# Optimization experiments

Hardware: AMD Instinct MI355X
Metric: run time of the kernel (lower is better)

Reference implementation:

```python
import jax, jax.numpy as jnp
import numpy as np

N, E, G = 50000, 800000, 64
F_IN, H, R, C = 64, 64, 3, 10


def setup_inputs() -> dict:
    key = jax.random.key(0)
    ks = jax.random.split(key, 16)
    s = 0.1
    return dict(
        x=jax.random.normal(ks[0], (N, F_IN), jnp.float32),
        edge_index=jax.random.randint(ks[1], (2, E), 0, N, dtype=jnp.int32),
        edge_type=jax.random.randint(ks[2], (E,), 0, R, dtype=jnp.int32),
        graph_batch=jnp.sort(jax.random.randint(ks[3], (N,), 0, G, dtype=jnp.int32)),
        # FiLMConv params (per-relation lin: bias=False; per-relation film: bias=True)
        film_lin_W=jax.random.normal(ks[4], (R, F_IN, H), jnp.float32) * s,
        film_film_W=jax.random.normal(ks[5], (R, F_IN, 2 * H), jnp.float32) * s,
        film_film_b=jnp.zeros((R, 2 * H), jnp.float32),
        skip_W=jax.random.normal(ks[6], (F_IN, H), jnp.float32) * s,
        skip_film_W=jax.random.normal(ks[7], (F_IN, 2 * H), jnp.float32) * s,
        skip_film_b=jnp.zeros((2 * H,), jnp.float32),
        # GATConv params (heads=1, concat=True, lin bias=False, final bias=True)
        gat_W=jax.random.normal(ks[8], (F_IN, H), jnp.float32) * s,
        gat_att_src=jax.random.normal(ks[9], (H,), jnp.float32) * s,
        gat_att_dst=jax.random.normal(ks[10], (H,), jnp.float32) * s,
        gat_b=jnp.zeros((H,), jnp.float32),
        # classifier MLP
        lin_W=jax.random.normal(ks[11], (4 * H, H), jnp.float32) * s,
        lin_b=jnp.zeros((H,), jnp.float32),
        fc_W=jax.random.normal(ks[12], (H, C), jnp.float32) * s,
        fc_b=jnp.zeros((C,), jnp.float32),
    )


def _film_conv(x, edge_index, edge_type, lin_W, film_W, film_b,
               skip_W, skip_film_W, skip_film_b):
    # PyG FiLMConv, aggr='mean' per relation, act=relu.
    n, r, h = x.shape[0], lin_W.shape[0], skip_W.shape[1]
    src, dst = edge_index[0], edge_index[1]
    fs = x @ skip_film_W + skip_film_b                  # [N,2H]; split -> (beta, gamma)
    out = jax.nn.relu(fs[:, h:] * (x @ skip_W) + fs[:, :h])
    xr = jnp.einsum('nd,rdh->rnh', x, lin_W)            # [R,N,H]
    fm = jnp.einsum('nd,rdh->rnh', x, film_W) + film_b[:, None, :]  # [R,N,2H]
    beta, gamma = fm[..., :h], fm[..., h:]
    # each edge uses its own relation's lin/film params
    msg = jax.nn.relu(gamma[edge_type, dst] * xr[edge_type, src] + beta[edge_type, dst])  # [E,H]
    seg = dst * r + edge_type                            # per-(node,relation) mean
    cnt = jax.ops.segment_sum(jnp.ones_like(msg[:, 0]), seg, num_segments=n * r)
    denom = jnp.maximum(cnt[seg], 1.0)
    agg = jax.ops.segment_sum(msg / denom[:, None], dst, num_segments=n)
    return out + agg


def _gat_conv(x, edge_index, W, att_src, att_dst, b):
    # PyG GATConv, heads=1, negative_slope=0.2, add_self_loops=True.
    n = x.shape[0]
    xp = x @ W                                           # [N,H]
    loop = jnp.arange(n, dtype=edge_index.dtype)
    src = jnp.concatenate([edge_index[0], loop])
    dst = jnp.concatenate([edge_index[1], loop])
    e = jax.nn.leaky_relu((xp @ att_src)[src] + (xp @ att_dst)[dst], 0.2)  # [E+N]
    m = jax.ops.segment_max(e, dst, num_segments=n)
    alpha = jnp.exp(e - m[dst])
    denom = jax.ops.segment_sum(alpha, dst, num_segments=n)
    alpha = alpha / denom[dst]
    return jax.ops.segment_sum(alpha[:, None] * xp[src], dst, num_segments=n) + b


def reference(x, edge_index, edge_type, graph_batch,
              film_lin_W, film_film_W, film_film_b, skip_W, skip_film_W, skip_film_b,
              gat_W, gat_att_src, gat_att_dst, gat_b,
              lin_W, lin_b, fc_W, fc_b):
    out1 = jax.nn.relu(_film_conv(x, edge_index, edge_type, film_lin_W, film_film_W,
                                  film_film_b, skip_W, skip_film_W, skip_film_b))
    out2 = jax.nn.relu(_gat_conv(x, edge_index, gat_W, gat_att_src, gat_att_dst, gat_b))
    feats = jnp.concatenate([out1, out2], axis=-1)       # [N,2H]
    g = G
    cnt = jax.ops.segment_sum(jnp.ones_like(feats[:, 0]), graph_batch, num_segments=g)
    mx = jax.ops.segment_max(feats, graph_batch, num_segments=g)
    mx = jnp.where(cnt[:, None] > 0, mx, 0.0)
    mean = jax.ops.segment_sum(feats, graph_batch, num_segments=g) / jnp.maximum(cnt, 1.0)[:, None]
    pooled = jnp.concatenate([mx, mean], axis=-1)        # [G,4H]
    hidden = jax.nn.relu(pooled @ lin_W + lin_b)         # dropout = identity (eval)
    logits = hidden @ fc_W + fc_b
    return jax.nn.log_softmax(logits, axis=-1)
```

## Files before the change

### kernel.cpp

```cpp
#include <hip/hip_runtime.h>
#include <hip/hip_bf16.h>

#define NN 50000
#define EE 800000
#define GG 64
#define RR 3
#define CC 10
#define RPL 16
#define CAP 96

typedef __attribute__((ext_vector_type(8))) short bf16x8;
typedef __attribute__((ext_vector_type(4))) float f32x4;

__device__ inline float leaky02(float x) { return x > 0.f ? x : 0.2f * x; }

__device__ inline void atomicMaxFPos(float* addr, float v) {
  atomicMax((int*)addr, __float_as_int(v));
}

__device__ inline unsigned short f2bf(float f) {
  __hip_bfloat16 b = __float2bfloat16(f);
  return *reinterpret_cast<unsigned short*>(&b);
}
__device__ inline float bf2f(unsigned short u) {
  return __uint_as_float(((unsigned int)u) << 16);
}

__global__ void scat_k(const int* __restrict__ ei, const int* __restrict__ et,
                       int* __restrict__ fill, int* __restrict__ sorted,
                       const float* __restrict__ skip_film_W,
                       const float* __restrict__ skip_W,
                       const float* __restrict__ film_lin_W,
                       const float* __restrict__ film_film_W,
                       const float* __restrict__ gat_W,
                       const float* __restrict__ skip_film_b,
                       const float* __restrict__ film_film_b,
                       unsigned short* __restrict__ Wt,
                       float* __restrict__ bias) {
  int b = blockIdx.x;
  if (b < 3125) {
    int e = b * 256 + threadIdx.x;
    int src = ei[e], dst = ei[EE + e], t = et[e];
    int slot = atomicAdd(&fill[dst], 1);
    if (slot < CAP) sorted[dst * CAP + slot] = src | (t << 20);
    return;
  }
  int idx = (b - 3125) * 256 + threadIdx.x;
  if (idx >= 832 * 64 + 832) return;
  if (idx >= 832 * 64) {
    int c = idx - 832 * 64;
    float bv = 0.f;
    if (c < 128) bv = skip_film_b[c];
    else if (c >= 384 && c < 768) bv = film_film_b[c - 384];
    bias[c] = bv;
    return;
  }
  int c = idx >> 6, k = idx & 63;
  float v;
  if (c < 128)      v = skip_film_W[k * 128 + c];
  else if (c < 192) v = skip_W[k * 64 + (c - 128)];
  else if (c < 384) { int cc = c - 192, r = cc >> 6, h = cc & 63;
                      v = film_lin_W[(r * 64 + k) * 64 + h]; }
  else if (c < 768) { int cc = c - 384, r = cc >> 7, j = cc & 127;
                      v = film_film_W[(r * 64 + k) * 128 + j]; }
  else              v = gat_W[k * 64 + (c - 768)];
  Wt[idx] = f2bf(v);
}

__global__ __launch_bounds__(256) void gemm_k(const float* __restrict__ X,
    const unsigned short* __restrict__ Wt, const float* __restrict__ bias,
    const float* __restrict__ att_src, const float* __restrict__ att_dst,
    unsigned short* __restrict__ Z, unsigned short* __restrict__ Ybg,
    unsigned short* __restrict__ S0b, float* __restrict__ as_,
    float* __restrict__ ad_) {
  __shared__ __align__(16) unsigned short As[64][72];
  __shared__ __align__(16) unsigned short Bs[128][72];
  const int tid = threadIdx.x;
  const int row0 = blockIdx.x * 64;

  {
    int r = tid >> 2, c0 = (tid & 3) * 16;
    int gr = row0 + r;
    ushort4 o0 = {0,0,0,0}, o1 = {0,0,0,0}, o2 = {0,0,0,0}, o3 = {0,0,0,0};
    if (gr < NN) {
      const float4* p = reinterpret_cast<const float4*>(X + (size_t)gr * 64 + c0);
      float4 v0 = p[0], v1 = p[1], v2 = p[2], v3 = p[3];
      o0 = {f2bf(v0.x), f2bf(v0.y), f2bf(v0.z), f2bf(v0.w)};
      o1 = {f2bf(v1.x), f2bf(v1.y), f2bf(v1.z), f2bf(v1.w)};
      o2 = {f2bf(v2.x), f2bf(v2.y), f2bf(v2.z), f2bf(v2.w)};
      o3 = {f2bf(v3.x), f2bf(v3.y), f2bf(v3.z), f2bf(v3.w)};
    }
    *reinterpret_cast<ushort4*>(&As[r][c0])      = o0;
    *reinterpret_cast<ushort4*>(&As[r][c0 + 4])  = o1;
    *reinterpret_cast<ushort4*>(&As[r][c0 + 8])  = o2;
    *reinterpret_cast<ushort4*>(&As[r][c0 + 12]) = o3;
  }
  __syncthreads();

  const int w = tid >> 6, lane = tid & 63;
  const int m = lane & 15, q = lane >> 4;
  bf16x8 a0 = *reinterpret_cast<const bf16x8*>(&As[16 * w + m][q * 8]);
  bf16x8 a1 = *reinterpret_cast<const bf16x8*>(&As[16 * w + m][32 + q * 8]);
  const int rbase = row0 + 16 * w + q * 4;

  unsigned short* Z0 = Z;
  unsigned short* Z1 = Z + (size_t)NN * 128;
  unsigned short* Z2 = Z + (size_t)NN * 256;

  f32x4 t0[8], t1[4], t6[4];

  for (int tile = 0; tile < 7; tile++) {
    __syncthreads();
    int col0 = tile * 128;
    int width = (tile == 6) ? 64 : 128;
    {
      int c = tid >> 1, half = (tid & 1) * 32;
      if (c < width) {
        int gc = col0 + c;
        const uint4* p = reinterpret_cast<const uint4*>(Wt + (size_t)gc * 64 + half);
        uint4 v0 = p[0], v1 = p[1], v2 = p[2], v3 = p[3];
        *reinterpret_cast<uint4*>(&Bs[c][half])      = v0;
        *reinterpret_cast<uint4*>(&Bs[c][half + 8])  = v1;
        *reinterpret_cast<uint4*>(&Bs[c][half + 16]) = v2;
        *reinterpret_cast<uint4*>(&Bs[c][half + 24]) = v3;
      }
    }
    __syncthreads();
    #pragma unroll
    for (int ct = 0; ct < 8; ct++) {
      if (tile == 6 && ct >= 4) continue;
      bf16x8 b0 = *reinterpret_cast<const bf16x8*>(&Bs[ct * 16 + m][q * 8]);
      bf16x8 b1 = *reinterpret_cast<const bf16x8*>(&Bs[ct * 16 + m][32 + q * 8]);
      f32x4 acc = {0.f, 0.f, 0.f, 0.f};
      acc = __builtin_amdgcn_mfma_f32_16x16x32_bf16(a0, b0, acc, 0, 0, 0);
      acc = __builtin_amdgcn_mfma_f32_16x16x32_bf16(a1, b1, acc, 0, 0, 0);
      if (tile == 0) { t0[ct] = acc; continue; }
      if (tile == 1 && ct < 4) { t1[ct] = acc; continue; }
      if (tile == 6) t6[ct] = acc;
      int colm = ct * 16 + m;
      float bv = (tile >= 3 && tile <= 5) ? bias[col0 + colm] : 0.f;
      #pragma unroll
      for (int rg = 0; rg < 4; rg++) {
        int gr = rbase + rg;
        if (gr >= NN) continue;
        float v = acc[rg];
        if (tile == 1) {
          Z0[(size_t)gr * 128 + colm] = f2bf(v);
        } else if (tile == 2) {
          if (ct < 4) Z1[(size_t)gr * 128 + 64 + colm] = f2bf(v);
          else        Z2[(size_t)gr * 128 + colm]      = f2bf(v);
        } else if (tile <= 5) {
          Ybg[(size_t)gr * 384 + (col0 - 384) + colm] = f2bf(v + bv);
        } else {
          unsigned short b16 = f2bf(v);
          Z0[(size_t)gr * 128 + colm] = b16;
          Z1[(size_t)gr * 128 + colm] = b16;
          Z2[(size_t)gr * 128 + colm] = b16;
        }
      }
    }
  }

  float pa[4] = {0.f, 0.f, 0.f, 0.f}, pd[4] = {0.f, 0.f, 0.f, 0.f};
  #pragma unroll
  for (int j = 0; j < 4; j++) {
    int h = 16 * j + m;
    float bb = bias[h];
    float bg = bias[64 + h];
    float asv = att_src[h];
    float adv = att_dst[h];
    #pragma unroll
    for (int rg = 0; rg < 4; rg++) {
      float so = fmaxf((t0[4 + j][rg] + bg) * t1[j][rg] + (t0[j][rg] + bb), 0.f);
      int gr = rbase + rg;
      if (gr < NN) S0b[(size_t)gr * 64 + h] = f2bf(so);
      pa[rg] += t6[j][rg] * asv;
      pd[rg] += t6[j][rg] * adv;
    }
  }
  #pragma unroll
  for (int ofs = 1; ofs < 16; ofs <<= 1) {
    #pragma unroll
    for (int rg = 0; rg < 4; rg++) {
      pa[rg] += __shfl_xor(pa[rg], ofs);
      pd[rg] += __shfl_xor(pd[rg], ofs);
    }
  }
  if (m == 0) {
    #pragma unroll
    for (int rg = 0; rg < 4; rg++) {
      int gr = rbase + rg;
      if (gr < NN) { as_[gr] = pa[rg]; ad_[gr] = pd[rg]; }
    }
  }
}

#define RPN 16

__global__ __launch_bounds__(256) void dst_k(const int* __restrict__ sorted,
    const int* __restrict__ fill, const unsigned short* __restrict__ Z,
    const unsigned short* __restrict__ Ybg,
    const unsigned short* __restrict__ S0b,
    const float* __restrict__ as_, const float* __restrict__ ad_,
    const float* __restrict__ gat_b, const int* __restrict__ gb,
    float* __restrict__ pmax, float* __restrict__ psum,
    int* __restrict__ gstart, int* __restrict__ gend) {
  __shared__ int s_wpk[8 * CAP];
  __shared__ __align__(16) unsigned short s_rows[64][128];
  __shared__ int s_deg[4], s_g[4];
  __shared__ float s_ad[4];
  float* s_val = (float*)&s_rows[0][0];

  int tid = threadIdx.x;
  int wid = tid >> 6, h = tid & 63;
  int n0 = blockIdx.x * 4;
  int n = n0 + wid;

  size_t rep = (size_t)(blockIdx.x & (RPL - 1)) * GG * 128;
  pmax += rep; psum += rep;

  if (h == 0) {
    int d = fill[n]; if (d > CAP) d = CAP;
    s_deg[wid] = d;
    s_g[wid] = gb[n];
    s_ad[wid] = ad_[n];
  }
  __syncthreads();

  for (int i = tid; i < 4 * CAP; i += 256) {
    int wd = i / CAP, j = i - wd * CAP;
    if (j < s_deg[wd]) {
      int pk = sorted[(size_t)(n0 + wd) * CAP + j];
      int s = pk & 0xFFFFF;
      float e = leaky02(as_[s] + s_ad[wd]);
      s_wpk[2 * i]     = pk;
      s_wpk[2 * i + 1] = __float_as_int(e);
    }
  }
  __syncthreads();

  int mydeg = s_deg[wid];
  float adn = s_ad[wid];
  float es = leaky02(as_[n] + adn);
  int base = wid * CAP;

  float e1 = -1e30f, e2 = -1e30f;
  int pk1 = -1, pk2 = -1;
  if (h < mydeg) {
    pk1 = s_wpk[2 * (base + h)];
    e1  = __int_as_float(s_wpk[2 * (base + h) + 1]);
  }
  if (h + 64 < mydeg) {
    pk2 = s_wpk[2 * (base + 64 + h)];
    e2  = __int_as_float(s_wpk[2 * (base + 64 + h) + 1]);
  }
  float mg = fmaxf(fmaxf(e1, e2), es);
  #pragma unroll
  for (int ofs = 1; ofs < 64; ofs <<= 1) mg = fmaxf(mg, __shfl_xor(mg, ofs));
  float w1 = (h < mydeg)      ? __expf(e1 - mg) : 0.f;
  float w2 = (h + 64 < mydeg) ? __expf(e2 - mg) : 0.f;
  if (h < mydeg)      s_wpk[2 * (base + h) + 1]      = __float_as_int(w1);
  if (h + 64 < mydeg) s_wpk[2 * (base + 64 + h) + 1] = __float_as_int(w2);
  float den = w1 + w2;
  #pragma unroll
  for (int ofs = 1; ofs < 64; ofs <<= 1) den += __shfl_xor(den, ofs);
  float ws = __expf(es - mg);
  den += ws;

  int t1v = pk1 >> 20, t2v = pk2 >> 20;
  int c0 = __popcll(__ballot(t1v == 0)) + __popcll(__ballot(t2v == 0));
  int c1 = __popcll(__ballot(t1v == 1)) + __popcll(__ballot(t2v == 1));
  int c2 = __popcll(__ballot(t1v == 2)) + __popcll(__ballot(t2v == 2));
  float i0 = 1.f / (float)(c0 > 1 ? c0 : 1);
  float i1 = 1.f / (float)(c1 > 1 ? c1 : 1);
  float i2 = 1.f / (float)(c2 > 1 ? c2 : 1);

  const unsigned short* ybg = Ybg + (size_t)n * 384;
  float b0p = bf2f(ybg[h])       * i0, g0p = bf2f(ybg[64 + h])  * i0;
  float b1p = bf2f(ybg[128 + h]) * i1, g1p = bf2f(ybg[192 + h]) * i1;
  float b2p = bf2f(ybg[256 + h]) * i2, g2p = bf2f(ybg[320 + h]) * i2;

  float S = ws * bf2f(Z[(size_t)n * 128 + h]);
  float f = 0.f;

  const int grp16 = tid >> 4, lane16 = tid & 15;
  int dmax = max(max(s_deg[0], s_deg[1]), max(s_deg[2], s_deg[3]));
  int rounds = (dmax + RPN - 1) / RPN;

  for (int r = 0; r < rounds; r++) {
    int e0 = r * RPN;
    #pragma unroll
    for (int k = 0; k < 4; k++) {
      int slot = grp16 + 16 * k;
      int wd = slot >> 4, j = slot & 15;
      int jj = e0 + j;
      if (jj < s_deg[wd]) {
        int pk = s_wpk[2 * (wd * CAP + jj)];
        int src = pk & 0xFFFFF;
        int t = pk >> 20;
        const unsigned short* row = Z + ((size_t)t * NN + src) * 128;
        uint4 v = *reinterpret_cast<const uint4*>(row + lane16 * 8);
        *reinterpret_cast<uint4*>(&s_rows[slot][lane16 * 8]) = v;
      }
    }
    __syncthreads();
    int cn = mydeg - e0; if (cn > RPN) cn = RPN;
    const int* wp = &s_wpk[2 * (base + e0)];
    const unsigned short* rowp = &s_rows[wid * RPN][0];
    for (int j = 0; j < cn; j++) {
      int pkj  = wp[2 * j];
      float wj = __int_as_float(wp[2 * j + 1]);
      int tj = pkj >> 20;
      float xp = bf2f(rowp[j * 128 + h]);
      float xr = bf2f(rowp[j * 128 + 64 + h]);
      S += wj * xp;
      float gt = tj == 0 ? g0p : (tj == 1 ? g1p : g2p);
      float bt = tj == 0 ? b0p : (tj == 1 ? b1p : b2p);
      f += fmaxf(gt * xr + bt, 0.f);
    }
    __syncthreads();
  }

  float o1 = fmaxf(bf2f(S0b[(size_t)n * 64 + h]) + f, 0.f);
  float o2 = fmaxf(S / den + gat_b[h], 0.f);

  s_val[wid * 128 + h]      = o1;
  s_val[wid * 128 + 64 + h] = o2;
  if (h == 0) {
    int g = s_g[wid];
    if (n == 0 || gb[n - 1] != g)      gstart[g] = n;
    if (n == NN - 1 || gb[n + 1] != g) gend[g] = n;
  }
  __syncthreads();
  if (tid < 128) {
    int fch = tid;
    int curg = s_g[0];
    float v0 = s_val[fch];
    float mx = v0, sm = v0;
    #pragma unroll
    for (int j = 1; j < 4; j++) {
      float v = s_val[j * 128 + fch];
      if (s_g[j] == curg) { mx = fmaxf(mx, v); sm += v; }
      else {
        atomicMaxFPos(&pmax[curg * 128 + fch], mx);
        atomicAdd(&psum[curg * 128 + fch], sm);
        curg = s_g[j]; mx = v; sm = v;
      }
    }
    atomicMaxFPos(&pmax[curg * 128 + fch], mx);
    atomicAdd(&psum[curg * 128 + fch], sm);
  }
}

__global__ __launch_bounds__(64) void head_k(const float* __restrict__ pmax,
    const float* __restrict__ psum, const int* __restrict__ gstart,
    const int* __restrict__ gend,
    const float* __restrict__ lin_W, const float* __restrict__ lin_b,
    const float* __restrict__ fc_W, const float* __restrict__ fc_b,
    float* __restrict__ out) {
  __shared__ float p[256];
  __shared__ float hid[64];
  __shared__ float lg[CC];
  __shared__ float lse;
  int g = blockIdx.x, t = threadIdx.x;
  int s = gstart[g], e = gend[g];
  int cnt = (s <= e && s < NN && s >= 0) ? (e - s + 1) : 0;
  float invc = 1.f / (float)(cnt > 1 ? cnt : 1);
  for (int i = t; i < 256; i += 64) {
    if (i < 128) {
      float mx = 0.f;
      for (int r = 0; r < RPL; r++)
        mx = fmaxf(mx, pmax[((size_t)r * GG + g) * 128 + i]);
      p[i] = mx;
    } else {
      int f = i - 128;
      float sm = 0.f;
      for (int r = 0; r < RPL; r++)
        sm += psum[((size_t)r * GG + g) * 128 + f];
      p[i] = sm * invc;
    }
  }
  __syncthreads();
  float acc = lin_b[t];
  for (int k = 0; k < 256; k++) acc += p[k] * lin_W[k * 64 + t];
  hid[t] = fmaxf(acc, 0.f);
  __syncthreads();
  if (t < CC) {
    float a = fc_b[t];
    for (int k = 0; k < 64; k++) a += hid[k] * fc_W[k * CC + t];
    lg[t] = a;
  }
  __syncthreads();
  if (t == 0) {
    float mx = lg[0];
    for (int i = 1; i < CC; i++) mx = fmaxf(mx, lg[i]);
    float sum = 0.f;
    for (int i = 0; i < CC; i++) sum += expf(lg[i] - mx);
    lse = mx + logf(sum);
  }
  __syncthreads();
  if (t < CC) out[g * CC + t] = lg[t] - lse;
}

extern "C" void kernel_launch(void* const* d_in, const int* in_sizes, int n_in,
                              void* d_out, int out_size, void* d_ws, size_t ws_size,
                              hipStream_t stream) {
  const float* x            = (const float*)d_in[0];
  const int*   edge_index   = (const int*)d_in[1];
  const int*   edge_type    = (const int*)d_in[2];
  const int*   graph_batch  = (const int*)d_in[3];
  const float* film_lin_W   = (const float*)d_in[4];
  const float* film_film_W  = (const float*)d_in[5];
  const float* film_film_b  = (const float*)d_in[6];
  const float* skip_W       = (const float*)d_in[7];
  const float* skip_film_W  = (const float*)d_in[8];
  const float* skip_film_b  = (const float*)d_in[9];
  const float* gat_W        = (const float*)d_in[10];
  const float* att_src      = (const float*)d_in[11];
  const float* att_dst      = (const float*)d_in[12];
  const float* gat_b        = (const float*)d_in[13];
  const float* lin_W        = (const float*)d_in[14];
  const float* lin_b        = (const float*)d_in[15];
  const float* fc_W         = (const float*)d_in[16];
  const float* fc_b         = (const float*)d_in[17];
  float* out                = (float*)d_out;

  float* ws = (float*)d_ws;
  const size_t N = NN, G = GG;
  size_t oZ      = 0;
  size_t oYbg    = N * 192;
  size_t oS0     = oYbg + N * 192;
  size_t oAs     = oS0 + N * 32;
  size_t oAd     = oAs + N;
  size_t oWt     = oAd + N;
  size_t oBias   = oWt + 832 * 32;
  size_t oPmax   = oBias + 832;
  size_t oPsum   = oPmax + (size_t)RPL * G * 128;
  size_t oGend   = oPsum + (size_t)RPL * G * 128;
  size_t oFill   = oGend + G;
  size_t oGstart = oFill + N;
  size_t oSorted = oGstart + G;

  unsigned short* Z   = (unsigned short*)(ws + oZ);
  unsigned short* Ybg = (unsigned short*)(ws + oYbg);
  unsigned short* S0b = (unsigned short*)(ws + oS0);
  float* as_    = ws + oAs;
  float* ad_    = ws + oAd;
  unsigned short* Wt  = (unsigned short*)(ws + oWt);
  float* bias   = ws + oBias;
  float* pmax   = ws + oPmax;
  float* psum   = ws + oPsum;
  int*   gend   = (int*)(ws + oGend);
  int*   fill   = (int*)(ws + oFill);
  int*   gstart = (int*)(ws + oGstart);
  int*   sorted = (int*)(ws + oSorted);

  size_t zeroFloats = oGstart - oPmax;
  hipMemsetAsync(pmax, 0, zeroFloats * sizeof(float), stream);

  scat_k<<<3125 + 210, 256, 0, stream>>>(edge_index, edge_type, fill, sorted,
      skip_film_W, skip_W, film_lin_W, film_film_W, gat_W,
      skip_film_b, film_film_b, Wt, bias);
  gemm_k<<<(NN + 63) / 64, 256, 0, stream>>>(x, Wt, bias, att_src, att_dst,
                                             Z, Ybg, S0b, as_, ad_);
  dst_k<<<NN / 4, 256, 0, stream>>>(sorted, fill, Z, Ybg, S0b, as_, ad_,
                                    gat_b, graph_batch, pmax, psum,
                                    gstart, gend);
  head_k<<<GG, 64, 0, stream>>>(pmax, psum, gstart, gend,
                                lin_W, lin_b, fc_W, fc_b, out);
}
```

Measured before the change: 248.6 us.

## Bucket edges by relation per destination and double-buffer neighbor row gathers

The edge scatter now bins each destination's incoming edges into three per-relation buckets of 32 slots, with a counter per (node, relation). Per-relation counts therefore come straight from those counters, which removes the ballot/popcount passes and the per-edge relation select in the inner loop. The dst kernel also double-buffers the shared-memory row tiles, loading the next round's neighbor rows into registers while the current round is processed, so there is one barrier per round instead of two. This doubles the shared staging buffer and adds register pressure. Capping each relation at 32 edges changes overflow behaviour compared with the single 96-slot cap.

```diff
diff --git a/kernel.cpp b/kernel.cpp
--- a/kernel.cpp
+++ b/kernel.cpp
@@ -27,7 +27,7 @@
 }
 
 __global__ void scat_k(const int* __restrict__ ei, const int* __restrict__ et,
-                       int* __restrict__ fill, int* __restrict__ sorted,
+                       int* __restrict__ fill4, int* __restrict__ sorted,
                        const float* __restrict__ skip_film_W,
                        const float* __restrict__ skip_W,
                        const float* __restrict__ film_lin_W,
@@ -41,8 +41,8 @@
   if (b < 3125) {
     int e = b * 256 + threadIdx.x;
     int src = ei[e], dst = ei[EE + e], t = et[e];
-    int slot = atomicAdd(&fill[dst], 1);
-    if (slot < CAP) sorted[dst * CAP + slot] = src | (t << 20);
+    int slot = atomicAdd(&fill4[dst * 4 + t], 1);
+    if (slot < 32) sorted[dst * 96 + t * 32 + slot] = src;
     return;
   }
   int idx = (b - 3125) * 256 + threadIdx.x;
@@ -198,128 +198,164 @@
 #define RPN 16
 
 __global__ __launch_bounds__(256) void dst_k(const int* __restrict__ sorted,
-    const int* __restrict__ fill, const unsigned short* __restrict__ Z,
+    const int* __restrict__ fill4, const unsigned short* __restrict__ Z,
     const unsigned short* __restrict__ Ybg,
     const unsigned short* __restrict__ S0b,
     const float* __restrict__ as_, const float* __restrict__ ad_,
     const float* __restrict__ gat_b, const int* __restrict__ gb,
     float* __restrict__ pmax, float* __restrict__ psum,
     int* __restrict__ gstart, int* __restrict__ gend) {
-  __shared__ int s_wpk[8 * CAP];
-  __shared__ __align__(16) unsigned short s_rows[64][128];
-  __shared__ int s_deg[4], s_g[4];
+  __shared__ int   s_pk[4][96];
+  __shared__ float s_w [4][96];
+  __shared__ int   s_d [4][4];
+  __shared__ int   s_g[4];
   __shared__ float s_ad[4];
-  float* s_val = (float*)&s_rows[0][0];
-
-  int tid = threadIdx.x;
-  int wid = tid >> 6, h = tid & 63;
-  int n0 = blockIdx.x * 4;
-  int n = n0 + wid;
+  __shared__ __align__(16) unsigned short s_rows[2][64][128];
+  float* s_val = (float*)&s_rows[0][0][0];
+
+  const int tid = threadIdx.x;
+  const int wid = tid >> 6, h = tid & 63;
+  const int n0 = blockIdx.x * 4;
+  const int n  = n0 + wid;
 
   size_t rep = (size_t)(blockIdx.x & (RPL - 1)) * GG * 128;
   pmax += rep; psum += rep;
 
-  if (h == 0) {
-    int d = fill[n]; if (d > CAP) d = CAP;
-    s_deg[wid] = d;
-    s_g[wid] = gb[n];
-    s_ad[wid] = ad_[n];
-  }
-  __syncthreads();
-
-  for (int i = tid; i < 4 * CAP; i += 256) {
-    int wd = i / CAP, j = i - wd * CAP;
-    if (j < s_deg[wd]) {
-      int pk = sorted[(size_t)(n0 + wd) * CAP + j];
-      int s = pk & 0xFFFFF;
-      float e = leaky02(as_[s] + s_ad[wd]);
-      s_wpk[2 * i]     = pk;
-      s_wpk[2 * i + 1] = __float_as_int(e);
-    }
-  }
-  __syncthreads();
-
-  int mydeg = s_deg[wid];
-  float adn = s_ad[wid];
+  if (tid < 16) {
+    int wd = tid >> 2, t = tid & 3;
+    if (t < 3) {
+      int d = fill4[(n0 + wd) * 4 + t];
+      s_d[wd][t] = d > 32 ? 32 : d;
+    } else {
+      s_g[wd]  = gb[n0 + wd];
+      s_ad[wd] = ad_[n0 + wd];
+    }
+  }
+  __syncthreads();
+
+  for (int i = tid; i < 512; i += 256) {
+    int wd = i >> 7, s = i & 127;
+    if (s < 96 && (s & 31) < s_d[wd][s >> 5]) {
+      int src = sorted[(size_t)(n0 + wd) * 96 + s];
+      s_pk[wd][s] = src;
+      s_w[wd][s]  = leaky02(as_[src] + s_ad[wd]);
+    }
+  }
+  __syncthreads();
+
+  const int d0 = s_d[wid][0], d1 = s_d[wid][1], d2 = s_d[wid][2];
+  const int sB = d0 + d1;
+  const int deg = sB + d2;
+  const float adn = s_ad[wid];
   float es = leaky02(as_[n] + adn);
-  int base = wid * CAP;
-
-  float e1 = -1e30f, e2 = -1e30f;
-  int pk1 = -1, pk2 = -1;
-  if (h < mydeg) {
-    pk1 = s_wpk[2 * (base + h)];
-    e1  = __int_as_float(s_wpk[2 * (base + h) + 1]);
-  }
-  if (h + 64 < mydeg) {
-    pk2 = s_wpk[2 * (base + 64 + h)];
-    e2  = __int_as_float(s_wpk[2 * (base + 64 + h) + 1]);
-  }
+
+  bool v1 = (h & 31) < ((h < 32) ? d0 : d1);
+  bool v2 = (h < 32) && (h < d2);
+  float e1 = v1 ? s_w[wid][h]      : -1e30f;
+  float e2 = v2 ? s_w[wid][64 + h] : -1e30f;
   float mg = fmaxf(fmaxf(e1, e2), es);
   #pragma unroll
   for (int ofs = 1; ofs < 64; ofs <<= 1) mg = fmaxf(mg, __shfl_xor(mg, ofs));
-  float w1 = (h < mydeg)      ? __expf(e1 - mg) : 0.f;
-  float w2 = (h + 64 < mydeg) ? __expf(e2 - mg) : 0.f;
-  if (h < mydeg)      s_wpk[2 * (base + h) + 1]      = __float_as_int(w1);
-  if (h + 64 < mydeg) s_wpk[2 * (base + 64 + h) + 1] = __float_as_int(w2);
+  float w1 = v1 ? __expf(e1 - mg) : 0.f;
+  float w2 = v2 ? __expf(e2 - mg) : 0.f;
+  if (v1) s_w[wid][h] = w1;
+  if (v2) s_w[wid][64 + h] = w2;
   float den = w1 + w2;
   #pragma unroll
   for (int ofs = 1; ofs < 64; ofs <<= 1) den += __shfl_xor(den, ofs);
   float ws = __expf(es - mg);
   den += ws;
 
-  int t1v = pk1 >> 20, t2v = pk2 >> 20;
-  int c0 = __popcll(__ballot(t1v == 0)) + __popcll(__ballot(t2v == 0));
-  int c1 = __popcll(__ballot(t1v == 1)) + __popcll(__ballot(t2v == 1));
-  int c2 = __popcll(__ballot(t1v == 2)) + __popcll(__ballot(t2v == 2));
-  float i0 = 1.f / (float)(c0 > 1 ? c0 : 1);
-  float i1 = 1.f / (float)(c1 > 1 ? c1 : 1);
-  float i2 = 1.f / (float)(c2 > 1 ? c2 : 1);
-
+  const float i0 = 1.f / (float)(d0 > 1 ? d0 : 1);
+  const float i1 = 1.f / (float)(d1 > 1 ? d1 : 1);
+  const float i2 = 1.f / (float)(d2 > 1 ? d2 : 1);
   const unsigned short* ybg = Ybg + (size_t)n * 384;
-  float b0p = bf2f(ybg[h])       * i0, g0p = bf2f(ybg[64 + h])  * i0;
-  float b1p = bf2f(ybg[128 + h]) * i1, g1p = bf2f(ybg[192 + h]) * i1;
-  float b2p = bf2f(ybg[256 + h]) * i2, g2p = bf2f(ybg[320 + h]) * i2;
+  const float b0p = bf2f(ybg[h])       * i0, g0p = bf2f(ybg[64 + h])  * i0;
+  const float b1p = bf2f(ybg[128 + h]) * i1, g1p = bf2f(ybg[192 + h]) * i1;
+  const float b2p = bf2f(ybg[256 + h]) * i2, g2p = bf2f(ybg[320 + h]) * i2;
 
   float S = ws * bf2f(Z[(size_t)n * 128 + h]);
   float f = 0.f;
 
   const int grp16 = tid >> 4, lane16 = tid & 15;
-  int dmax = max(max(s_deg[0], s_deg[1]), max(s_deg[2], s_deg[3]));
+  int kA[4], kB[4], kD[4];
+  #pragma unroll
+  for (int k = 0; k < 4; k++) {
+    kA[k] = s_d[k][0];
+    kB[k] = kA[k] + s_d[k][1];
+    kD[k] = kB[k] + s_d[k][2];
+  }
+  int dmax = max(max(kD[0], kD[1]), max(kD[2], kD[3]));
   int rounds = (dmax + RPN - 1) / RPN;
 
-  for (int r = 0; r < rounds; r++) {
-    int e0 = r * RPN;
+  uint4 rv[4];
+  auto GLOAD = [&](int e0) {
     #pragma unroll
     for (int k = 0; k < 4; k++) {
-      int slot = grp16 + 16 * k;
-      int wd = slot >> 4, j = slot & 15;
-      int jj = e0 + j;
-      if (jj < s_deg[wd]) {
-        int pk = s_wpk[2 * (wd * CAP + jj)];
-        int src = pk & 0xFFFFF;
-        int t = pk >> 20;
-        const unsigned short* row = Z + ((size_t)t * NN + src) * 128;
-        uint4 v = *reinterpret_cast<const uint4*>(row + lane16 * 8);
-        *reinterpret_cast<uint4*>(&s_rows[slot][lane16 * 8]) = v;
-      }
-    }
+      int jj = e0 + grp16;
+      if (jj < kD[k]) {
+        int slot = jj < kA[k] ? jj
+                 : (jj < kB[k] ? 32 + jj - kA[k] : 64 + jj - kB[k]);
+        int src = s_pk[k][slot];
+        int t = slot >> 5;
+        rv[k] = *reinterpret_cast<const uint4*>(
+            Z + ((size_t)t * NN + src) * 128 + lane16 * 8);
+      }
+    }
+  };
+  auto WRITE = [&](int buf, int e0) {
+    #pragma unroll
+    for (int k = 0; k < 4; k++) {
+      int jj = e0 + grp16;
+      if (jj < kD[k])
+        *reinterpret_cast<uint4*>(&s_rows[buf][16 * k + grp16][lane16 * 8]) = rv[k];
+    }
+  };
+
+  int cur = 0;
+  if (rounds > 0) {
+    GLOAD(0);
+    WRITE(0, 0);
     __syncthreads();
-    int cn = mydeg - e0; if (cn > RPN) cn = RPN;
-    const int* wp = &s_wpk[2 * (base + e0)];
-    const unsigned short* rowp = &s_rows[wid * RPN][0];
-    for (int j = 0; j < cn; j++) {
-      int pkj  = wp[2 * j];
-      float wj = __int_as_float(wp[2 * j + 1]);
-      int tj = pkj >> 20;
-      float xp = bf2f(rowp[j * 128 + h]);
-      float xr = bf2f(rowp[j * 128 + 64 + h]);
-      S += wj * xp;
-      float gt = tj == 0 ? g0p : (tj == 1 ? g1p : g2p);
-      float bt = tj == 0 ? b0p : (tj == 1 ? b1p : b2p);
-      f += fmaxf(gt * xr + bt, 0.f);
-    }
-    __syncthreads();
-  }
+    for (int r = 0; r < rounds; r++) {
+      int e0 = r * RPN;
+      GLOAD(e0 + RPN);
+      const unsigned short* rowp = &s_rows[cur][wid * RPN][0];
+      int hi0 = min(e0 + RPN, d0);
+      for (int i = e0; i < hi0; i++) {
+        float wj = s_w[wid][i];
+        int sr = i - e0;
+        float xp = bf2f(rowp[sr * 128 + h]);
+        float xr = bf2f(rowp[sr * 128 + 64 + h]);
+        S += wj * xp;
+        f += fmaxf(g0p * xr + b0p, 0.f);
+      }
+      int lo1 = max(e0, d0), hi1 = min(e0 + RPN, sB);
+      for (int i = lo1; i < hi1; i++) {
+        float wj = s_w[wid][32 + i - d0];
+        int sr = i - e0;
+        float xp = bf2f(rowp[sr * 128 + h]);
+        float xr = bf2f(rowp[sr * 128 + 64 + h]);
+        S += wj * xp;
+        f += fmaxf(g1p * xr + b1p, 0.f);
+      }
+      int lo2 = max(e0, sB), hi2 = min(e0 + RPN, deg);
+      for (int i = lo2; i < hi2; i++) {
+        float wj = s_w[wid][64 + i - sB];
+        int sr = i - e0;
+        float xp = bf2f(rowp[sr * 128 + h]);
+        float xr = bf2f(rowp[sr * 128 + 64 + h]);
+        S += wj * xp;
+        f += fmaxf(g2p * xr + b2p, 0.f);
+      }
+      if (r + 1 < rounds) {
+        WRITE(cur ^ 1, e0 + RPN);
+        __syncthreads();
+        cur ^= 1;
+      }
+    }
+  }
+  __syncthreads();
 
   float o1 = fmaxf(bf2f(S0b[(size_t)n * 64 + h]) + f, 0.f);
   float o2 = fmaxf(S / den + gat_b[h], 0.f);
@@ -438,7 +474,7 @@
   size_t oPsum   = oPmax + (size_t)RPL * G * 128;
   size_t oGend   = oPsum + (size_t)RPL * G * 128;
   size_t oFill   = oGend + G;
-  size_t oGstart = oFill + N;
+  size_t oGstart = oFill + N * 4;
   size_t oSorted = oGstart + G;
 
   unsigned short* Z   = (unsigned short*)(ws + oZ);
@@ -451,19 +487,19 @@
   float* pmax   = ws + oPmax;
   float* psum   = ws + oPsum;
   int*   gend   = (int*)(ws + oGend);
-  int*   fill   = (int*)(ws + oFill);
+  int*   fill4  = (int*)(ws + oFill);
   int*   gstart = (int*)(ws + oGstart);
   int*   sorted = (int*)(ws + oSorted);
 
   size_t zeroFloats = oGstart - oPmax;
   hipMemsetAsync(pmax, 0, zeroFloats * sizeof(float), stream);
 
-  scat_k<<<3125 + 210, 256, 0, stream>>>(edge_index, edge_type, fill, sorted,
+  scat_k<<<3125 + 210, 256, 0, stream>>>(edge_index, edge_type, fill4, sorted,
       skip_film_W, skip_W, film_lin_W, film_film_W, gat_W,
       skip_film_b, film_film_b, Wt, bias);
   gemm_k<<<(NN + 63) / 64, 256, 0, stream>>>(x, Wt, bias, att_src, att_dst,
                                              Z, Ybg, S0b, as_, ad_);
-  dst_k<<<NN / 4, 256, 0, stream>>>(sorted, fill, Z, Ybg, S0b, as_, ad_,
+  dst_k<<<NN / 4, 256, 0, stream>>>(sorted, fill4, Z, Ybg, S0b, as_, ad_,
                                     gat_b, graph_batch, pmax, psum,
                                     gstart, gend);
   head_k<<<GG, 64, 0, stream>>>(pmax, psum, gstart, gend,
```

Result: slower. 336.7 us (+35.4%).
